# Kernel optimization log

Measured on AMD Instinct MI355X. Metric: run time of the kernel, lower is better.

The kernel has to match this reference:

```python
import jax, jax.numpy as jnp
import numpy as np

B, N, M, D, KV, H = 4, 1024, 1024, 1024, 1024, 16
HD = D // H


def setup_inputs() -> dict:
    key = jax.random.key(0)
    ks = jax.random.split(key, 9)
    s = 0.02
    return {
        "query": jax.random.normal(ks[0], (B, N, D), jnp.float32),
        "key_value": jax.random.normal(ks[1], (B, M, KV), jnp.float32),
        "mask": jax.random.bernoulli(ks[2], 0.1, (B, M)),  # True = masked out
        "Wq": jax.random.normal(ks[3], (D, D), jnp.float32) * s,
        "bq": jnp.zeros((D,), jnp.float32),
        "Wkv": jax.random.normal(ks[4], (KV, 2 * D), jnp.float32) * s,
        "bkv": jnp.zeros((2 * D,), jnp.float32),
        "Wp": jax.random.normal(ks[5], (D, 2), jnp.float32) * s,
        "bp": jnp.zeros((2,), jnp.float32),
    }


def reference(query, key_value, mask, Wq, bq, Wkv, bkv, Wp, bp):
    b, n, d = query.shape
    m = key_value.shape[1]
    scale = HD ** (-0.5)
    # projections
    queries = (query @ Wq + bq).reshape(b, n, H, HD)
    kv = (key_value @ Wkv + bkv).reshape(b, m, 2, H, HD)
    keys, values = kv[:, :, 0], kv[:, :, 1]
    # scores in bnmh layout (as the original einsum)
    attention = jnp.einsum('bnhd,bmhd->bnmh', queries, keys) * scale
    # mask [b,m] -> unsqueeze(1) -> [b,1,m] -> unsqueeze(3) -> [b,1,m,1]
    attention = jnp.where(mask[:, None, :, None], -jnp.inf, attention)
    attention = jax.nn.softmax(attention, axis=2)
    outputs = jnp.einsum('bnmh,bmhd->bnhd', attention, values).reshape(b, n, d)
    outputs = outputs @ Wp + bp
    return outputs, attention
```

## Files before the change

### kernel.cpp

```cpp
#include <hip/hip_runtime.h>

typedef unsigned short u16;
typedef unsigned int u32;
typedef __bf16 bf16x8 __attribute__((ext_vector_type(8)));
typedef float f32x4 __attribute__((ext_vector_type(4)));

#define MFMA16 __builtin_amdgcn_mfma_f32_16x16x32_bf16


__device__ __forceinline__ float b2f(u16 u){ u32 x = ((u32)u)<<16; float f; __builtin_memcpy(&f,&x,4); return f; }
__device__ __forceinline__ u16 f2b(float f){ u32 x; __builtin_memcpy(&x,&f,4); return (u16)((x + 0x7fffu + ((x>>16)&1u)) >> 16); }
__device__ __forceinline__ bf16x8 ldf(const u16* p){ uint4 v = *(const uint4*)p; return __builtin_bit_cast(bf16x8, v); }
__device__ __forceinline__ u32 pk(u16 a, u16 b){ return (u32)a | ((u32)b<<16); }

__device__ __forceinline__ void stage16(const u16* g, u16* l) {
  __builtin_amdgcn_global_load_lds(
      (const __attribute__((address_space(1))) void*)g,
      (__attribute__((address_space(3))) void*)l, 16, 0, 0);
}

__device__ __forceinline__ uint4 ld8(const void* base, size_t off, int f32) {
  if (f32) {
    const float* p = (const float*)base + off;
    f32x4 a = *(const f32x4*)p;
    f32x4 b = *(const f32x4*)(p + 4);
    uint4 r;
    r.x = pk(f2b(a[0]), f2b(a[1]));
    r.y = pk(f2b(a[2]), f2b(a[3]));
    r.z = pk(f2b(b[0]), f2b(b[1]));
    r.w = pk(f2b(b[2]), f2b(b[3]));
    return r;
  }
  return *(const uint4*)((const u16*)base + off);
}
__device__ __forceinline__ float lds1(const void* base, size_t off, int f32) {
  return f32 ? ((const float*)base)[off] : b2f(((const u16*)base)[off]);
}

__global__ __launch_bounds__(256) void detect_dtype(const u32* __restrict__ q, int* __restrict__ flag) {
  __shared__ int cnt;
  if (threadIdx.x == 0) cnt = 0;
  __syncthreads();
  int c = 0;
#pragma unroll
  for (int i = 0; i < 4; i++) {
    u32 w = q[threadIdx.x + i*256];
    u32 e = (w >> 7) & 0xFFu;
    c += (e >= 100u && e <= 140u) ? 1 : 0;
  }
#pragma unroll
  for (int m = 1; m <= 32; m <<= 1) c += __shfl_xor(c, m);
  if ((threadIdx.x & 63) == 0) atomicAdd(&cnt, c);
  __syncthreads();
  if (threadIdx.x == 0) flag[0] = (cnt < 512) ? 1 : 0;
}

__global__ __launch_bounds__(1024) void mask_convert(const void* __restrict__ mraw,
                                                     float* __restrict__ maskF) {
  __shared__ u32 orv;
  const int t = threadIdx.x;
  if (t == 0) orv = 0u;
  __syncthreads();
  u32 o = ((const u32*)mraw)[t];
#pragma unroll
  for (int m = 1; m <= 32; m <<= 1) o |= __shfl_xor(o, m);
  if ((t & 63) == 0) atomicOr(&orv, o);
  __syncthreads();
  const u32 orall = orv;
  int mode;
  if ((orall & ~0x01010101u) == 0u) mode = (orall <= 1u) ? 0 : 1;
  else if (orall & 0x0000FF80u)     mode = 2;
  else                              mode = 3;
  const float NEGINF = -__builtin_inff();
#pragma unroll
  for (int i = t; i < 4096; i += 1024) {
    bool mm;
    if      (mode == 0) mm = ((const int*)mraw)[i] != 0;
    else if (mode == 1) mm = ((const unsigned char*)mraw)[i] != 0;
    else if (mode == 2) mm = ((const u16*)mraw)[i] != 0;
    else                mm = ((const float*)mraw)[i] != 0.f;
    maskF[i] = mm ? NEGINF : 0.f;
  }
}

__global__ __launch_bounds__(256) void to_bf16(const void* __restrict__ in, const int* __restrict__ flag,
                                               u16* __restrict__ out) {
  const int f32 = flag[0];
  const size_t idx = ((size_t)blockIdx.x*256 + threadIdx.x)*8;
  *(uint4*)(out + idx) = ld8(in, idx, f32);
}

__global__ __launch_bounds__(256) void transpose_w(const void* __restrict__ in, const int* __restrict__ flag,
                                                   u16* __restrict__ out, int R, int C) {
  __shared__ u16 tile[64][72];
  const int f32 = flag[0];
  const int t = threadIdx.x;
  const int c0 = blockIdx.x*64, r0 = blockIdx.y*64;
  const int lr = t >> 2, cs = (t & 3)*16;
#pragma unroll
  for (int i=0;i<2;i++)
    *(uint4*)&tile[lr][cs + i*8] = ld8(in, (size_t)(r0 + lr)*C + c0 + cs + i*8, f32);
  __syncthreads();
  const int c = t >> 2, rs = (t & 3)*16;
  u16 v[16];
#pragma unroll
  for (int j=0;j<16;j++) v[j] = tile[rs + j][c];
  uint4 u0 = { pk(v[0],v[1]), pk(v[2],v[3]), pk(v[4],v[5]), pk(v[6],v[7]) };
  uint4 u1 = { pk(v[8],v[9]), pk(v[10],v[11]), pk(v[12],v[13]), pk(v[14],v[15]) };
  u16* op = out + (size_t)(c0 + c)*R + r0 + rs;
  *(uint4*)op = u0;
  *(uint4*)(op + 8) = u1;
}

__global__ __launch_bounds__(256) void gemm_nt(const u16* __restrict__ A, const u16* __restrict__ Bt,
                                               const void* __restrict__ bias, const int* __restrict__ flag,
                                               u16* __restrict__ C, int Mdim, int Ndim, int Kdim) {
  __shared__ u16 As[128][64];
  __shared__ u16 Bs[128][64];
  const int f32 = flag[0];
  const int tid = threadIdx.x, l = tid & 63, w = tid >> 6;
  const int n0 = blockIdx.x * 128, m0 = blockIdx.y * 128;
  const int wr = (w & 1) * 64, wc = (w >> 1) * 64;
  const int lr = l & 15, lg = l >> 4;
  f32x4 acc[4][4];
#pragma unroll
  for (int i=0;i<4;i++)
#pragma unroll
    for (int j=0;j<4;j++) acc[i][j] = (f32x4){0.f,0.f,0.f,0.f};
  const int srow = l >> 3;
  const int scol = (l & 7) * 8;
  const u16* Ab = A  + (size_t)m0 * Kdim;
  const u16* Bb = Bt + (size_t)n0 * Kdim;
  for (int k0 = 0; k0 < Kdim; k0 += 64) {
    __syncthreads();
#pragma unroll
    for (int i = 0; i < 4; i++) {
      const int seg = i*4 + w;
      stage16(Ab + (size_t)(seg*8 + srow)*Kdim + k0 + scol, &As[seg*8][0]);
      stage16(Bb + (size_t)(seg*8 + srow)*Kdim + k0 + scol, &Bs[seg*8][0]);
    }
    __syncthreads();
    bf16x8 af[4][2], bfr[4][2];
#pragma unroll
    for (int rt=0; rt<4; rt++) {
      af[rt][0] = ldf(&As[wr + rt*16 + lr][lg*8]);
      af[rt][1] = ldf(&As[wr + rt*16 + lr][32 + lg*8]);
    }
#pragma unroll
    for (int ct=0; ct<4; ct++) {
      bfr[ct][0] = ldf(&Bs[wc + ct*16 + lr][lg*8]);
      bfr[ct][1] = ldf(&Bs[wc + ct*16 + lr][32 + lg*8]);
    }
#pragma unroll
    for (int rt=0; rt<4; rt++)
#pragma unroll
      for (int ct=0; ct<4; ct++) {
        acc[rt][ct] = MFMA16(af[rt][0], bfr[ct][0], acc[rt][ct], 0,0,0);
        acc[rt][ct] = MFMA16(af[rt][1], bfr[ct][1], acc[rt][ct], 0,0,0);
      }
  }
#pragma unroll
  for (int ct=0; ct<4; ct++) {
    const int col = n0 + wc + ct*16 + lr;
    const float bv = lds1(bias, col, f32);
#pragma unroll
    for (int rt=0; rt<4; rt++)
#pragma unroll
      for (int r=0; r<4; r++) {
        const int row = m0 + wr + rt*16 + lg*4 + r;
        C[(size_t)row * Ndim + col] = f2b(acc[rt][ct][r] + bv);
      }
  }
}

__global__ __launch_bounds__(256) void build_vt(const u16* __restrict__ KVb, u16* __restrict__ Vt) {
  __shared__ u16 tile[64][72];
  const int t = threadIdx.x;
  const int m0 = blockIdx.x*64, h = blockIdx.y, b = blockIdx.z;
  const int mr = t >> 2, cs = (t & 3)*16;
  const u16* src = KVb + (size_t)(b*1024 + m0 + mr)*2048 + 1024 + h*64;
#pragma unroll
  for (int i=0;i<2;i++)
    *(uint4*)&tile[mr][cs + i*8] = *(const uint4*)(src + cs + i*8);
  __syncthreads();
  const int hd = t >> 2, ms = (t & 3)*16;
  u16 v[16];
#pragma unroll
  for (int j=0;j<16;j++) v[j] = tile[ms + j][hd];
  uint4 u0 = { pk(v[0],v[1]), pk(v[2],v[3]), pk(v[4],v[5]), pk(v[6],v[7]) };
  uint4 u1 = { pk(v[8],v[9]), pk(v[10],v[11]), pk(v[12],v[13]), pk(v[14],v[15]) };
  u16* op = Vt + (size_t)((b*16 + h)*64 + hd)*1024 + m0 + ms;
  *(uint4*)op = u0;
  *(uint4*)(op + 8) = u1;
}

__global__ __launch_bounds__(256) void attn_kern(const u16* __restrict__ Qb, const u16* __restrict__ KVb,
                                                 const u16* __restrict__ Vt, const float* __restrict__ maskF,
                                                 u16* __restrict__ Pbuf, u16* __restrict__ Obuf,
                                                 float* __restrict__ Sc, float* __restrict__ Fin) {
  __shared__ u16 Ks[128][72];
  __shared__ u16 Vts[64][136];
  __shared__ u16 Ps[4][16][136];
  __shared__ float mlds[128];
  const int tid = threadIdx.x, l = tid & 63, w = tid >> 6;
  const int lr = l & 15, lg = l >> 4;
  const int n0 = blockIdx.x * 64, h = blockIdx.y, b = blockIdx.z;
  const float NEGINF = -__builtin_inff();
  const float scale2 = 0.125f * 1.44269504088896f;

  bf16x8 qf[2];
  {
    const u16* Qsrc = Qb + (size_t)(b*1024 + n0 + 16*w + lr)*1024 + h*64 + lg*8;
    qf[0] = ldf(Qsrc);
    qf[1] = ldf(Qsrc + 32);
  }
  float mrow[4] = {NEGINF,NEGINF,NEGINF,NEGINF};
  float lrow[4] = {0.f,0.f,0.f,0.f};
  f32x4 oacc[4];
#pragma unroll
  for (int vt=0; vt<4; vt++) oacc[vt] = (f32x4){0.f,0.f,0.f,0.f};

  const int ksr = tid >> 1, kss = (tid & 1)*32;
  const u16* Kbase = KVb + (size_t)(b*1024)*2048 + h*64;
  const u16* Vbase = Vt + (size_t)((b*16 + h)*64)*1024;
  const int vsr = tid >> 2, vss = (tid & 3)*32;

  for (int c = 0; c < 8; c++) {
    const int m0 = c*128;
    __syncthreads();
#pragma unroll
    for (int i=0;i<4;i++)
      *(uint4*)&Ks[ksr][kss + i*8] = *(const uint4*)(Kbase + (size_t)(m0 + ksr)*2048 + kss + i*8);
#pragma unroll
    for (int i=0;i<4;i++)
      *(uint4*)&Vts[vsr][vss + i*8] = *(const uint4*)(Vbase + (size_t)vsr*1024 + m0 + vss + i*8);
    if (tid < 128) mlds[tid] = maskF[b*1024 + m0 + tid];
    __syncthreads();
    f32x4 sa[8];
#pragma unroll
    for (int ct=0; ct<8; ct++) {
      sa[ct] = (f32x4){0.f,0.f,0.f,0.f};
      bf16x8 k0 = ldf(&Ks[ct*16 + lr][lg*8]);
      bf16x8 k1 = ldf(&Ks[ct*16 + lr][32 + lg*8]);
      sa[ct] = MFMA16(qf[0], k0, sa[ct], 0,0,0);
      sa[ct] = MFMA16(qf[1], k1, sa[ct], 0,0,0);
    }
    float cmax[4] = {NEGINF,NEGINF,NEGINF,NEGINF};
#pragma unroll
    for (int ct=0; ct<8; ct++) {
      const float mv = mlds[ct*16 + lr];
#pragma unroll
      for (int r=0;r<4;r++) {
        float s = fmaf(sa[ct][r], scale2, mv);
        sa[ct][r] = s;
        cmax[r] = fmaxf(cmax[r], s);
      }
    }
    float al[4];
#pragma unroll
    for (int r=0;r<4;r++) {
#pragma unroll
      for (int m = 1; m <= 8; m <<= 1) cmax[r] = fmaxf(cmax[r], __shfl_xor(cmax[r], m));
      const float mnew = fmaxf(mrow[r], cmax[r]);
      al[r] = exp2f(fmaxf(mrow[r] - mnew, -1000.f));
      float se = 0.f;
#pragma unroll
      for (int ct=0; ct<8; ct++) {
        float p = exp2f(fmaxf(sa[ct][r] - mnew, -1000.f));
        sa[ct][r] = p;
        se += p;
      }
#pragma unroll
      for (int m = 1; m <= 8; m <<= 1) se += __shfl_xor(se, m);
      lrow[r] = lrow[r] * al[r] + se;
      mrow[r] = mnew;
      if (lr == 0)
        Sc[(((size_t)b*1024 + n0 + 16*w + lg*4 + r)*16 + h)*8 + c] = mnew;
    }
#pragma unroll
    for (int ct=0; ct<8; ct++)
#pragma unroll
      for (int r=0;r<4;r++)
        Ps[w][lg*4 + r][ct*16 + lr] = f2b(sa[ct][r]);
    {
      const int pr = l >> 2, psg = (l & 3) * 32;
      u16* gp = Pbuf + (size_t)((b*16 + h)*1024 + n0 + 16*w + pr)*1024 + m0 + psg;
#pragma unroll
      for (int i=0;i<4;i++)
        *(uint4*)(gp + i*8) = *(const uint4*)&Ps[w][pr][psg + i*8];
    }
#pragma unroll
    for (int vt=0; vt<4; vt++)
#pragma unroll
      for (int r=0;r<4;r++) oacc[vt][r] *= al[r];
    bf16x8 pa[4];
#pragma unroll
    for (int t=0;t<4;t++) pa[t] = ldf(&Ps[w][lr][t*32 + lg*8]);
#pragma unroll
    for (int vt=0; vt<4; vt++) {
#pragma unroll
      for (int t=0;t<4;t++) {
        bf16x8 bv = ldf(&Vts[vt*16 + lr][t*32 + lg*8]);
        oacc[vt] = MFMA16(pa[t], bv, oacc[vt], 0,0,0);
      }
    }
  }
  float rinv[4];
#pragma unroll
  for (int r=0;r<4;r++) rinv[r] = (lrow[r] > 0.f) ? 1.f / lrow[r] : 0.f;
#pragma unroll
  for (int vt=0; vt<4; vt++)
#pragma unroll
    for (int r=0;r<4;r++) {
      const int row = b*1024 + n0 + 16*w + lg*4 + r;
      const int col = h*64 + vt*16 + lr;
      Obuf[(size_t)row*1024 + col] = f2b(oacc[vt][r] * rinv[r]);
    }
  if (lr == 0) {
#pragma unroll
    for (int r=0;r<4;r++) {
      const size_t fo = (((size_t)b*1024 + n0 + 16*w + lg*4 + r)*16 + h)*2;
      Fin[fo]   = mrow[r];
      Fin[fo+1] = rinv[r];
    }
  }
}

__global__ __launch_bounds__(256) void transpose_p(const u16* __restrict__ Pbuf,
                                                   const float* __restrict__ Sc,
                                                   const float* __restrict__ Fin,
                                                   float* __restrict__ out) {
  __shared__ u16 t2[16][1024];
  __shared__ float slut[128];
  const int t = threadIdx.x;
  const int n = blockIdx.x, b = blockIdx.y;
  const int h = t >> 4, sg = (t & 15)*64;
  const u16* src = Pbuf + (size_t)((b*16 + h)*1024 + n)*1024 + sg;
#pragma unroll
  for (int i=0;i<8;i++)
    *(uint4*)&t2[h][sg + i*8] = *(const uint4*)(src + i*8);
  if (t < 128) {
    const int hh = t >> 3, cc = t & 7;
    const size_t base = ((size_t)b*1024 + n)*16 + hh;
    const float mc = Sc[base*8 + cc];
    const float mf = Fin[base*2];
    const float ri = Fin[base*2 + 1];
    slut[t] = exp2f(fmaxf(mc - mf, -1000.f)) * ri;
  }
  __syncthreads();
  float* dst = out + (size_t)(b*1024 + n)*16384;
#pragma unroll
  for (int mi=0; mi<4; mi++) {
    const int m = t + mi*256;
    const int c = m >> 7;
#pragma unroll
    for (int q=0; q<4; q++) {
      f32x4 v;
#pragma unroll
      for (int j=0; j<4; j++) v[j] = b2f(t2[q*4 + j][m]) * slut[(q*4 + j)*8 + c];
      *(f32x4*)(dst + (size_t)m*16 + q*4) = v;
    }
  }
}

__global__ __launch_bounds__(256) void proj_out_k(const u16* __restrict__ Obuf, const void* __restrict__ Wp,
                                                  const void* __restrict__ bp, const int* __restrict__ flag,
                                                  float* __restrict__ out0) {
  const int f32 = flag[0];
  const int l = threadIdx.x & 63, w = threadIdx.x >> 6;
  const int row = blockIdx.x*4 + w;
  const u16* op = Obuf + (size_t)row*1024 + l*16;
  float d0 = 0.f, d1 = 0.f;
#pragma unroll
  for (int j=0;j<16;j++) {
    const float o = b2f(op[j]);
    d0 = fmaf(o, lds1(Wp, (size_t)(l*16 + j)*2,     f32), d0);
    d1 = fmaf(o, lds1(Wp, (size_t)(l*16 + j)*2 + 1, f32), d1);
  }
#pragma unroll
  for (int m=1; m<=32; m<<=1) { d0 += __shfl_xor(d0, m); d1 += __shfl_xor(d1, m); }
  if (l == 0) {
    out0[row*2]   = d0 + lds1(bp, 0, f32);
    out0[row*2+1] = d1 + lds1(bp, 1, f32);
  }
}

extern "C" void kernel_launch(void* const* d_in, const int* in_sizes, int n_in,
                              void* d_out, int out_size, void* d_ws, size_t ws_size,
                              hipStream_t stream) {
  const void* query     = d_in[0];
  const void* key_value = d_in[1];
  const void* mask      = d_in[2];
  const void* Wq        = d_in[3];
  const void* bq        = d_in[4];
  const void* Wkv       = d_in[5];
  const void* bkv       = d_in[6];
  const void* Wp        = d_in[7];
  const void* bp        = d_in[8];
  float* out0     = (float*)d_out;
  float* attn_out = (float*)d_out + 8192;

  char* ws = (char*)d_ws;
  u16*   WqT   = (u16*)(ws);
  u16*   WkvT  = (u16*)(ws + (2u<<20));
  u16*   Qb    = (u16*)(ws + (6u<<20));
  u16*   KVb   = (u16*)(ws + (14u<<20));
  u16*   Vt    = (u16*)(ws + (30u<<20));
  u16*   Obuf  = (u16*)(ws + (38u<<20));
  float* maskF = (float*)(ws + (46u<<20));
  int*   flag  = (int*)(ws + (46u<<20) + 16384);
  u16*   Pbuf  = (u16*)(ws + (47u<<20));
  float* Sc    = (float*)(ws + (175u<<20));
  float* Fin   = (float*)(ws + (177u<<20));
  u16*   Qc    = (u16*)(ws + (47u<<20));
  u16*   KVc   = (u16*)(ws + (55u<<20));

  detect_dtype<<<1, 256, 0, stream>>>((const u32*)query, flag);
  mask_convert<<<1, 1024, 0, stream>>>(mask, maskF);
  to_bf16<<<2048, 256, 0, stream>>>(query,     flag, Qc);
  to_bf16<<<2048, 256, 0, stream>>>(key_value, flag, KVc);
  transpose_w<<<dim3(16,16), 256, 0, stream>>>(Wq, flag, WqT, 1024, 1024);
  transpose_w<<<dim3(32,16), 256, 0, stream>>>(Wkv, flag, WkvT, 1024, 2048);
  gemm_nt<<<dim3(8,32),  256, 0, stream>>>(Qc,  WqT,  bq,  flag, Qb,  4096, 1024, 1024);
  gemm_nt<<<dim3(16,32), 256, 0, stream>>>(KVc, WkvT, bkv, flag, KVb, 4096, 2048, 1024);
  build_vt<<<dim3(16,16,4), 256, 0, stream>>>(KVb, Vt);
  attn_kern<<<dim3(16,16,4), 256, 0, stream>>>(Qb, KVb, Vt, maskF, Pbuf, Obuf, Sc, Fin);
  transpose_p<<<dim3(1024,4), 256, 0, stream>>>(Pbuf, Sc, Fin, attn_out);
  proj_out_k<<<dim3(1024), 256, 0, stream>>>(Obuf, Wp, bp, flag, out0);
}
```

Measured before the change: 545.2 us.

## Double-buffer GEMM LDS tiles, prefetch attention K/V in registers, merge bf16 converts

The projection GEMM now keeps two LDS buffers and issues the global-to-LDS loads for the next K tile while MFMAs run on the current one, with one barrier per iteration. The attention kernel loads the next chunk's K, V and mask into registers before computing on the current chunk, so global load latency overlaps with compute. The two bf16 conversion launches are merged into one launch. This costs extra LDS in the GEMM and more registers in the attention kernel, which may lower occupancy.

```diff
diff --git a/kernel.cpp b/kernel.cpp
--- a/kernel.cpp
+++ b/kernel.cpp
@@ -83,11 +83,17 @@
   }
 }
 
-__global__ __launch_bounds__(256) void to_bf16(const void* __restrict__ in, const int* __restrict__ flag,
-                                               u16* __restrict__ out) {
+__global__ __launch_bounds__(256) void to_bf16_2(const void* __restrict__ q, const void* __restrict__ kv,
+                                                 const int* __restrict__ flag,
+                                                 u16* __restrict__ outq, u16* __restrict__ outkv) {
   const int f32 = flag[0];
-  const size_t idx = ((size_t)blockIdx.x*256 + threadIdx.x)*8;
-  *(uint4*)(out + idx) = ld8(in, idx, f32);
+  if (blockIdx.x < 2048) {
+    const size_t idx = ((size_t)blockIdx.x*256 + threadIdx.x)*8;
+    *(uint4*)(outq + idx) = ld8(q, idx, f32);
+  } else {
+    const size_t idx = ((size_t)(blockIdx.x - 2048)*256 + threadIdx.x)*8;
+    *(uint4*)(outkv + idx) = ld8(kv, idx, f32);
+  }
 }
 
 __global__ __launch_bounds__(256) void transpose_w(const void* __restrict__ in, const int* __restrict__ flag,
@@ -115,8 +121,8 @@
 __global__ __launch_bounds__(256) void gemm_nt(const u16* __restrict__ A, const u16* __restrict__ Bt,
                                                const void* __restrict__ bias, const int* __restrict__ flag,
                                                u16* __restrict__ C, int Mdim, int Ndim, int Kdim) {
-  __shared__ u16 As[128][64];
-  __shared__ u16 Bs[128][64];
+  __shared__ u16 As[2][128][64];
+  __shared__ u16 Bs[2][128][64];
   const int f32 = flag[0];
   const int tid = threadIdx.x, l = tid & 63, w = tid >> 6;
   const int n0 = blockIdx.x * 128, m0 = blockIdx.y * 128;
@@ -131,25 +137,35 @@
   const int scol = (l & 7) * 8;
   const u16* Ab = A  + (size_t)m0 * Kdim;
   const u16* Bb = Bt + (size_t)n0 * Kdim;
-  for (int k0 = 0; k0 < Kdim; k0 += 64) {
-    __syncthreads();
-#pragma unroll
-    for (int i = 0; i < 4; i++) {
-      const int seg = i*4 + w;
-      stage16(Ab + (size_t)(seg*8 + srow)*Kdim + k0 + scol, &As[seg*8][0]);
-      stage16(Bb + (size_t)(seg*8 + srow)*Kdim + k0 + scol, &Bs[seg*8][0]);
-    }
-    __syncthreads();
+  const int nt = Kdim >> 6;
+#pragma unroll
+  for (int i = 0; i < 4; i++) {
+    const int seg = i*4 + w;
+    stage16(Ab + (size_t)(seg*8 + srow)*Kdim + scol, &As[0][seg*8][0]);
+    stage16(Bb + (size_t)(seg*8 + srow)*Kdim + scol, &Bs[0][seg*8][0]);
+  }
+  __syncthreads();
+  for (int t = 0; t < nt; t++) {
+    const int pp = t & 1;
+    if (t + 1 < nt) {
+      const int k1 = (t + 1) << 6;
+#pragma unroll
+      for (int i = 0; i < 4; i++) {
+        const int seg = i*4 + w;
+        stage16(Ab + (size_t)(seg*8 + srow)*Kdim + k1 + scol, &As[pp^1][seg*8][0]);
+        stage16(Bb + (size_t)(seg*8 + srow)*Kdim + k1 + scol, &Bs[pp^1][seg*8][0]);
+      }
+    }
     bf16x8 af[4][2], bfr[4][2];
 #pragma unroll
     for (int rt=0; rt<4; rt++) {
-      af[rt][0] = ldf(&As[wr + rt*16 + lr][lg*8]);
-      af[rt][1] = ldf(&As[wr + rt*16 + lr][32 + lg*8]);
+      af[rt][0] = ldf(&As[pp][wr + rt*16 + lr][lg*8]);
+      af[rt][1] = ldf(&As[pp][wr + rt*16 + lr][32 + lg*8]);
     }
 #pragma unroll
     for (int ct=0; ct<4; ct++) {
-      bfr[ct][0] = ldf(&Bs[wc + ct*16 + lr][lg*8]);
-      bfr[ct][1] = ldf(&Bs[wc + ct*16 + lr][32 + lg*8]);
+      bfr[ct][0] = ldf(&Bs[pp][wc + ct*16 + lr][lg*8]);
+      bfr[ct][1] = ldf(&Bs[pp][wc + ct*16 + lr][32 + lg*8]);
     }
 #pragma unroll
     for (int rt=0; rt<4; rt++)
@@ -158,6 +174,7 @@
         acc[rt][ct] = MFMA16(af[rt][0], bfr[ct][0], acc[rt][ct], 0,0,0);
         acc[rt][ct] = MFMA16(af[rt][1], bfr[ct][1], acc[rt][ct], 0,0,0);
       }
+    __syncthreads();
   }
 #pragma unroll
   for (int ct=0; ct<4; ct++) {
@@ -225,17 +242,33 @@
   const u16* Vbase = Vt + (size_t)((b*16 + h)*64)*1024;
   const int vsr = tid >> 2, vss = (tid & 3)*32;
 
+  uint4 kreg[4], vreg[4];
+  float mreg;
+#pragma unroll
+  for (int i=0;i<4;i++) {
+    kreg[i] = *(const uint4*)(Kbase + (size_t)ksr*2048 + kss + i*8);
+    vreg[i] = *(const uint4*)(Vbase + (size_t)vsr*1024 + vss + i*8);
+  }
+  mreg = (tid < 128) ? maskF[b*1024 + tid] : 0.f;
+
   for (int c = 0; c < 8; c++) {
-    const int m0 = c*128;
     __syncthreads();
 #pragma unroll
-    for (int i=0;i<4;i++)
-      *(uint4*)&Ks[ksr][kss + i*8] = *(const uint4*)(Kbase + (size_t)(m0 + ksr)*2048 + kss + i*8);
-#pragma unroll
-    for (int i=0;i<4;i++)
-      *(uint4*)&Vts[vsr][vss + i*8] = *(const uint4*)(Vbase + (size_t)vsr*1024 + m0 + vss + i*8);
-    if (tid < 128) mlds[tid] = maskF[b*1024 + m0 + tid];
+    for (int i=0;i<4;i++) {
+      *(uint4*)&Ks[ksr][kss + i*8] = kreg[i];
+      *(uint4*)&Vts[vsr][vss + i*8] = vreg[i];
+    }
+    if (tid < 128) mlds[tid] = mreg;
     __syncthreads();
+    if (c < 7) {
+      const int m1 = (c + 1) * 128;
+#pragma unroll
+      for (int i=0;i<4;i++) {
+        kreg[i] = *(const uint4*)(Kbase + (size_t)(m1 + ksr)*2048 + kss + i*8);
+        vreg[i] = *(const uint4*)(Vbase + (size_t)vsr*1024 + m1 + vss + i*8);
+      }
+      mreg = (tid < 128) ? maskF[b*1024 + m1 + tid] : 0.f;
+    }
     f32x4 sa[8];
 #pragma unroll
     for (int ct=0; ct<8; ct++) {
@@ -284,7 +317,7 @@
         Ps[w][lg*4 + r][ct*16 + lr] = f2b(sa[ct][r]);
     {
       const int pr = l >> 2, psg = (l & 3) * 32;
-      u16* gp = Pbuf + (size_t)((b*16 + h)*1024 + n0 + 16*w + pr)*1024 + m0 + psg;
+      u16* gp = Pbuf + (size_t)((b*16 + h)*1024 + n0 + 16*w + pr)*1024 + c*128 + psg;
 #pragma unroll
       for (int i=0;i<4;i++)
         *(uint4*)(gp + i*8) = *(const uint4*)&Ps[w][pr][psg + i*8];
@@ -417,8 +450,7 @@
 
   detect_dtype<<<1, 256, 0, stream>>>((const u32*)query, flag);
   mask_convert<<<1, 1024, 0, stream>>>(mask, maskF);
-  to_bf16<<<2048, 256, 0, stream>>>(query,     flag, Qc);
-  to_bf16<<<2048, 256, 0, stream>>>(key_value, flag, KVc);
+  to_bf16_2<<<4096, 256, 0, stream>>>(query, key_value, flag, Qc, KVc);
   transpose_w<<<dim3(16,16), 256, 0, stream>>>(Wq, flag, WqT, 1024, 1024);
   transpose_w<<<dim3(32,16), 256, 0, stream>>>(Wkv, flag, WkvT, 1024, 2048);
   gemm_nt<<<dim3(8,32),  256, 0, stream>>>(Qc,  WqT,  bq,  flag, Qb,  4096, 1024, 1024);
```

Result: slower. 595.8 us (+9.3%).

## Merge prep, conversion, transpose and projection GEMM launches; fix transpose_p LDS conflicts

Applied to the files above, without the earlier changes.

Pairs of independent kernels (dtype detect and mask convert, the two bf16 conversions, the two weight transposes, the Q and KV projection GEMMs) are each merged into one launch that picks its work by block index. This cuts launch count and lets the smaller Q work share the GPU with the larger KV work instead of running alone. transpose_p pads the LDS tile row to 1036 and changes its load and store mapping so each thread writes one 16-byte chunk of a 64-byte row segment, aimed at fewer bank conflicts and better-coalesced stores. The risk is extra branching per block and slightly more LDS per block.

```diff
diff --git a/kernel.cpp b/kernel.cpp
--- a/kernel.cpp
+++ b/kernel.cpp
@@ -37,65 +37,71 @@
   return f32 ? ((const float*)base)[off] : b2f(((const u16*)base)[off]);
 }
 
-__global__ __launch_bounds__(256) void detect_dtype(const u32* __restrict__ q, int* __restrict__ flag) {
-  __shared__ int cnt;
-  if (threadIdx.x == 0) cnt = 0;
-  __syncthreads();
-  int c = 0;
-#pragma unroll
-  for (int i = 0; i < 4; i++) {
-    u32 w = q[threadIdx.x + i*256];
-    u32 e = (w >> 7) & 0xFFu;
-    c += (e >= 100u && e <= 140u) ? 1 : 0;
-  }
-#pragma unroll
-  for (int m = 1; m <= 32; m <<= 1) c += __shfl_xor(c, m);
-  if ((threadIdx.x & 63) == 0) atomicAdd(&cnt, c);
-  __syncthreads();
-  if (threadIdx.x == 0) flag[0] = (cnt < 512) ? 1 : 0;
-}
-
-__global__ __launch_bounds__(1024) void mask_convert(const void* __restrict__ mraw,
-                                                     float* __restrict__ maskF) {
-  __shared__ u32 orv;
+__global__ __launch_bounds__(256) void fused_prep(const u32* __restrict__ q, const void* __restrict__ mraw,
+                                                  int* __restrict__ flag, float* __restrict__ maskF) {
   const int t = threadIdx.x;
-  if (t == 0) orv = 0u;
-  __syncthreads();
-  u32 o = ((const u32*)mraw)[t];
-#pragma unroll
-  for (int m = 1; m <= 32; m <<= 1) o |= __shfl_xor(o, m);
-  if ((t & 63) == 0) atomicOr(&orv, o);
-  __syncthreads();
-  const u32 orall = orv;
-  int mode;
-  if ((orall & ~0x01010101u) == 0u) mode = (orall <= 1u) ? 0 : 1;
-  else if (orall & 0x0000FF80u)     mode = 2;
-  else                              mode = 3;
-  const float NEGINF = -__builtin_inff();
-#pragma unroll
-  for (int i = t; i < 4096; i += 1024) {
-    bool mm;
-    if      (mode == 0) mm = ((const int*)mraw)[i] != 0;
-    else if (mode == 1) mm = ((const unsigned char*)mraw)[i] != 0;
-    else if (mode == 2) mm = ((const u16*)mraw)[i] != 0;
-    else                mm = ((const float*)mraw)[i] != 0.f;
-    maskF[i] = mm ? NEGINF : 0.f;
-  }
-}
-
-__global__ __launch_bounds__(256) void to_bf16(const void* __restrict__ in, const int* __restrict__ flag,
-                                               u16* __restrict__ out) {
+  if (blockIdx.x == 0) {
+    __shared__ int cnt;
+    if (t == 0) cnt = 0;
+    __syncthreads();
+    int c = 0;
+#pragma unroll
+    for (int i = 0; i < 4; i++) {
+      u32 w = q[t + i*256];
+      u32 e = (w >> 7) & 0xFFu;
+      c += (e >= 100u && e <= 140u) ? 1 : 0;
+    }
+#pragma unroll
+    for (int m = 1; m <= 32; m <<= 1) c += __shfl_xor(c, m);
+    if ((t & 63) == 0) atomicAdd(&cnt, c);
+    __syncthreads();
+    if (t == 0) flag[0] = (cnt < 512) ? 1 : 0;
+  } else {
+    __shared__ u32 orv;
+    if (t == 0) orv = 0u;
+    __syncthreads();
+    u32 o = 0u;
+#pragma unroll
+    for (int i = 0; i < 4; i++) o |= ((const u32*)mraw)[t + i*256];
+#pragma unroll
+    for (int m = 1; m <= 32; m <<= 1) o |= __shfl_xor(o, m);
+    if ((t & 63) == 0) atomicOr(&orv, o);
+    __syncthreads();
+    const u32 orall = orv;
+    int mode;
+    if ((orall & ~0x01010101u) == 0u) mode = (orall <= 1u) ? 0 : 1;
+    else if (orall & 0x0000FF80u)     mode = 2;
+    else                              mode = 3;
+    const float NEGINF = -__builtin_inff();
+    for (int i = t; i < 4096; i += 256) {
+      bool mm;
+      if      (mode == 0) mm = ((const int*)mraw)[i] != 0;
+      else if (mode == 1) mm = ((const unsigned char*)mraw)[i] != 0;
+      else if (mode == 2) mm = ((const u16*)mraw)[i] != 0;
+      else                mm = ((const float*)mraw)[i] != 0.f;
+      maskF[i] = mm ? NEGINF : 0.f;
+    }
+  }
+}
+
+__global__ __launch_bounds__(256) void to_bf16_2(const void* __restrict__ q, const void* __restrict__ kv,
+                                                 const int* __restrict__ flag,
+                                                 u16* __restrict__ outq, u16* __restrict__ outkv) {
   const int f32 = flag[0];
-  const size_t idx = ((size_t)blockIdx.x*256 + threadIdx.x)*8;
-  *(uint4*)(out + idx) = ld8(in, idx, f32);
-}
-
-__global__ __launch_bounds__(256) void transpose_w(const void* __restrict__ in, const int* __restrict__ flag,
-                                                   u16* __restrict__ out, int R, int C) {
+  if (blockIdx.x < 2048) {
+    const size_t idx = ((size_t)blockIdx.x*256 + threadIdx.x)*8;
+    *(uint4*)(outq + idx) = ld8(q, idx, f32);
+  } else {
+    const size_t idx = ((size_t)(blockIdx.x - 2048)*256 + threadIdx.x)*8;
+    *(uint4*)(outkv + idx) = ld8(kv, idx, f32);
+  }
+}
+
+__device__ __forceinline__ void transpose_w_body(const void* in, int f32, u16* out,
+                                                 int R, int C, int bx, int by) {
   __shared__ u16 tile[64][72];
-  const int f32 = flag[0];
   const int t = threadIdx.x;
-  const int c0 = blockIdx.x*64, r0 = blockIdx.y*64;
+  const int c0 = bx*64, r0 = by*64;
   const int lr = t >> 2, cs = (t & 3)*16;
 #pragma unroll
   for (int i=0;i<2;i++)
@@ -112,14 +118,20 @@
   *(uint4*)(op + 8) = u1;
 }
 
-__global__ __launch_bounds__(256) void gemm_nt(const u16* __restrict__ A, const u16* __restrict__ Bt,
-                                               const void* __restrict__ bias, const int* __restrict__ flag,
-                                               u16* __restrict__ C, int Mdim, int Ndim, int Kdim) {
+__global__ __launch_bounds__(256) void transpose_w2(const void* __restrict__ Wq, const void* __restrict__ Wkv,
+                                                    const int* __restrict__ flag,
+                                                    u16* __restrict__ WqT, u16* __restrict__ WkvT) {
+  const int f32 = flag[0];
+  if (blockIdx.x < 16) transpose_w_body(Wq,  f32, WqT,  1024, 1024, blockIdx.x,      blockIdx.y);
+  else                 transpose_w_body(Wkv, f32, WkvT, 1024, 2048, blockIdx.x - 16, blockIdx.y);
+}
+
+__device__ __forceinline__ void gemm_body(const u16* A, const u16* Bt, const void* bias, int f32,
+                                          u16* C, int Ndim, int Kdim, int bx, int by) {
   __shared__ u16 As[128][64];
   __shared__ u16 Bs[128][64];
-  const int f32 = flag[0];
   const int tid = threadIdx.x, l = tid & 63, w = tid >> 6;
-  const int n0 = blockIdx.x * 128, m0 = blockIdx.y * 128;
+  const int n0 = bx * 128, m0 = by * 128;
   const int wr = (w & 1) * 64, wc = (w >> 1) * 64;
   const int lr = l & 15, lg = l >> 4;
   f32x4 acc[4][4];
@@ -171,6 +183,23 @@
         C[(size_t)row * Ndim + col] = f2b(acc[rt][ct][r] + bv);
       }
   }
+}
+
+__global__ __launch_bounds__(256) void gemm_fused(const u16* __restrict__ Qc, const u16* __restrict__ WqT,
+                                                  const void* __restrict__ bq,
+                                                  const u16* __restrict__ KVc, const u16* __restrict__ WkvT,
+                                                  const void* __restrict__ bkv,
+                                                  const int* __restrict__ flag,
+                                                  u16* __restrict__ Qb, u16* __restrict__ KVb) {
+  const int f32 = flag[0];
+  const bool isQ = blockIdx.x < 8;
+  const u16* A    = isQ ? Qc  : KVc;
+  const u16* Bt   = isQ ? WqT : WkvT;
+  const void* bia = isQ ? bq  : bkv;
+  u16* C          = isQ ? Qb  : KVb;
+  const int Ndim  = isQ ? 1024 : 2048;
+  const int bx    = isQ ? blockIdx.x : blockIdx.x - 8;
+  gemm_body(A, Bt, bia, f32, C, Ndim, 1024, bx, blockIdx.y);
 }
 
 __global__ __launch_bounds__(256) void build_vt(const u16* __restrict__ KVb, u16* __restrict__ Vt) {
@@ -330,15 +359,15 @@
                                                    const float* __restrict__ Sc,
                                                    const float* __restrict__ Fin,
                                                    float* __restrict__ out) {
-  __shared__ u16 t2[16][1024];
+  __shared__ u16 t2[16][1036];
   __shared__ float slut[128];
   const int t = threadIdx.x;
   const int n = blockIdx.x, b = blockIdx.y;
-  const int h = t >> 4, sg = (t & 15)*64;
-  const u16* src = Pbuf + (size_t)((b*16 + h)*1024 + n)*1024 + sg;
+  const int h = t >> 4, k = t & 15;
+  const u16* src = Pbuf + (size_t)((b*16 + h)*1024 + n)*1024;
 #pragma unroll
   for (int i=0;i<8;i++)
-    *(uint4*)&t2[h][sg + i*8] = *(const uint4*)(src + i*8);
+    *(uint4*)&t2[h][k*8 + i*128] = *(const uint4*)(src + k*8 + i*128);
   if (t < 128) {
     const int hh = t >> 3, cc = t & 7;
     const size_t base = ((size_t)b*1024 + n)*16 + hh;
@@ -349,17 +378,18 @@
   }
   __syncthreads();
   float* dst = out + (size_t)(b*1024 + n)*16384;
-#pragma unroll
-  for (int mi=0; mi<4; mi++) {
-    const int m = t + mi*256;
+  const int mq = t >> 2, hq = t & 3;
+#pragma unroll
+  for (int mi=0; mi<16; mi++) {
+    const int m = mq + mi*64;
     const int c = m >> 7;
-#pragma unroll
-    for (int q=0; q<4; q++) {
-      f32x4 v;
-#pragma unroll
-      for (int j=0; j<4; j++) v[j] = b2f(t2[q*4 + j][m]) * slut[(q*4 + j)*8 + c];
-      *(f32x4*)(dst + (size_t)m*16 + q*4) = v;
-    }
+    f32x4 v;
+#pragma unroll
+    for (int j=0; j<4; j++) {
+      const int hh = hq*4 + j;
+      v[j] = b2f(t2[hh][m]) * slut[hh*8 + c];
+    }
+    *(f32x4*)(dst + (size_t)m*16 + hq*4) = v;
   }
 }
 
@@ -415,14 +445,10 @@
   u16*   Qc    = (u16*)(ws + (47u<<20));
   u16*   KVc   = (u16*)(ws + (55u<<20));
 
-  detect_dtype<<<1, 256, 0, stream>>>((const u32*)query, flag);
-  mask_convert<<<1, 1024, 0, stream>>>(mask, maskF);
-  to_bf16<<<2048, 256, 0, stream>>>(query,     flag, Qc);
-  to_bf16<<<2048, 256, 0, stream>>>(key_value, flag, KVc);
-  transpose_w<<<dim3(16,16), 256, 0, stream>>>(Wq, flag, WqT, 1024, 1024);
-  transpose_w<<<dim3(32,16), 256, 0, stream>>>(Wkv, flag, WkvT, 1024, 2048);
-  gemm_nt<<<dim3(8,32),  256, 0, stream>>>(Qc,  WqT,  bq,  flag, Qb,  4096, 1024, 1024);
-  gemm_nt<<<dim3(16,32), 256, 0, stream>>>(KVc, WkvT, bkv, flag, KVb, 4096, 2048, 1024);
+  fused_prep<<<2, 256, 0, stream>>>((const u32*)query, mask, flag, maskF);
+  to_bf16_2<<<4096, 256, 0, stream>>>(query, key_value, flag, Qc, KVc);
+  transpose_w2<<<dim3(48,16), 256, 0, stream>>>(Wq, Wkv, flag, WqT, WkvT);
+  gemm_fused<<<dim3(24,32), 256, 0, stream>>>(Qc, WqT, bq, KVc, WkvT, bkv, flag, Qb, KVb);
   build_vt<<<dim3(16,16,4), 256, 0, stream>>>(KVb, Vt);
   attn_kern<<<dim3(16,16,4), 256, 0, stream>>>(Qb, KVb, Vt, maskF, Pbuf, Obuf, Sc, Fin);
   transpose_p<<<dim3(1024,4), 256, 0, stream>>>(Pbuf, Sc, Fin, attn_out);
```

Measured after the change: 518.9 us. 1.05x faster.
